# Optimization experiments

Hardware: AMD Instinct MI355X
Metric: run time of the kernel (lower is better)

Reference implementation:

```python
import jax, jax.numpy as jnp
import numpy as np

B, T, D = 8, 2048, 1024

def _xavier(key, shape):
    fan_in, fan_out = shape[1], shape[0]
    limit = float(np.sqrt(6.0 / (fan_in + fan_out)))
    return jax.random.uniform(key, shape, jnp.float32, -limit, limit)

def setup_inputs() -> dict:
    key = jax.random.key(0)
    ks = jax.random.split(key, 6)
    x = jax.random.normal(ks[0], (B, T, D), jnp.float32)
    return {
        "x": x,
        "h0": jnp.zeros((B, D), jnp.float32),
        "W_in": _xavier(ks[1], (D, D)),      # in_proj.weight [d_inner, dim]
        "W_alpha": _xavier(ks[2], (D, D)),
        "d_alpha": jnp.full((D,), 0.1, jnp.float32),
        "b_alpha": jnp.full((D,), 2.0, jnp.float32),
        "W_x": _xavier(ks[3], (D, D)),
        "b_v": jnp.zeros((D,), jnp.float32),
        "W_out": _xavier(ks[4], (D, D)),     # out_proj.weight [dim, d_inner]
    }

def _silu(u):
    return u * jax.nn.sigmoid(u)

def reference(x, h0, W_in, W_alpha, d_alpha, b_alpha, W_x, b_v, W_out):
    # in_proj + SiLU: [B,T,D]
    x_proj = _silu(jnp.einsum('btd,ed->bte', x, W_in))
    # to [T,B,D] for the scan
    x_rnn = jnp.transpose(x_proj, (1, 0, 2))
    # precompute per-step gate/value GEMM contributions (as in torch ref)
    alpha_x = jnp.einsum('tbd,ed->tbe', x_rnn, W_alpha)          # [T,B,D]
    v_all = jnp.tanh(jnp.einsum('tbd,ed->tbe', x_rnn, W_x) + b_v)  # [T,B,D]

    def step(h_prev, inputs):
        ax_t, v_t = inputs
        alpha = jax.nn.sigmoid(ax_t + d_alpha * h_prev + b_alpha)
        h_new = alpha * h_prev + (1.0 - alpha) * v_t
        out_t = h_new * _silu(h_new)
        return h_new, out_t

    h_final, cell_out = jax.lax.scan(step, h0, (alpha_x, v_all))  # cell_out: [T,B,D]
    cell_out = jnp.transpose(cell_out, (1, 0, 2))                 # [B,T,D]
    output = jnp.einsum('btd,ed->bte', cell_out, W_out)
    return output, h_final
```

## Files before the change

kernel.cpp:

```cpp
#include <hip/hip_runtime.h>
#include <hip/hip_bf16.h>

typedef __attribute__((ext_vector_type(8))) short short8;
typedef __attribute__((ext_vector_type(4))) short short4v;
typedef __attribute__((ext_vector_type(4))) float f32x4;

#define Dk 1024
#define TT 2048
#define BB 8
#define MROWS (BB * TT)
#define LOG2E 1.44269504088896f

#if defined(__has_builtin)
#if __has_builtin(__builtin_amdgcn_rcpf)
#define FAST_RCP(x) __builtin_amdgcn_rcpf(x)
#endif
#if __has_builtin(__builtin_amdgcn_exp2f)
#define FAST_EXP2(x) __builtin_amdgcn_exp2f(x)
#endif
#endif
#ifndef FAST_RCP
#define FAST_RCP(x) (1.f / (x))
#endif
#ifndef FAST_EXP2
#define FAST_EXP2(x) exp2f(x)
#endif

__device__ __forceinline__ void gload_lds16(const void* g, void* l) {
    __builtin_amdgcn_global_load_lds(
        (const __attribute__((address_space(1))) void*)g,
        (__attribute__((address_space(3))) void*)l, 16, 0, 0);
}

__device__ __forceinline__ float sigmoidf_fast(float x) {
    return FAST_RCP(1.f + FAST_EXP2(-x * LOG2E));
}

__device__ __forceinline__ unsigned short bf16_bits(float x) {
    union { __hip_bfloat16 h; unsigned short u; } c;
    c.h = __float2bfloat16(x);
    return c.u;
}

__global__ __launch_bounds__(256)
void cvt_all(const float* __restrict__ x,
             const float* __restrict__ w0, const float* __restrict__ w1,
             const float* __restrict__ w2, const float* __restrict__ w3,
             __hip_bfloat16* __restrict__ xo,
             __hip_bfloat16* __restrict__ o0, __hip_bfloat16* __restrict__ o1,
             __hip_bfloat16* __restrict__ o2, __hip_bfloat16* __restrict__ o3)
{
    const int bid = blockIdx.x;
    const float* in;
    __hip_bfloat16* out;
    int base;
    if (bid < 16384) {
        in = x; out = xo; base = bid * 1024;
    } else {
        const int wbid  = bid - 16384;
        const int which = wbid >> 10;
        in  = which == 0 ? w0 : which == 1 ? w1 : which == 2 ? w2 : w3;
        out = which == 0 ? o0 : which == 1 ? o1 : which == 2 ? o2 : o3;
        base = (wbid & 1023) * 1024;
    }
    const int i = base + threadIdx.x * 4;
    const float4 v = *(const float4*)(in + i);
    __hip_bfloat16 tmp[4];
    tmp[0] = __float2bfloat16(v.x);
    tmp[1] = __float2bfloat16(v.y);
    tmp[2] = __float2bfloat16(v.z);
    tmp[3] = __float2bfloat16(v.w);
    *(short4v*)(out + i) = *(const short4v*)tmp;
}

template<int EPI>
__global__ __launch_bounds__(512, 2)
void gemm256(const __hip_bfloat16* __restrict__ A,
             const __hip_bfloat16* __restrict__ Bw,
             const float* __restrict__ bias,
             void* __restrict__ CoutV)
{
    __shared__ __align__(16) char lds[3 * 32768];

    const int tid  = threadIdx.x;
    const int bid  = blockIdx.x;
    const int nbid = (bid & 7) * 32 + (bid >> 3);
    const int tn   = nbid & 3;
    const int tm   = nbid >> 2;
    const int lane = tid & 63;
    const int w    = tid >> 6;
    const int wm   = w >> 2;
    const int wn   = w & 3;
    const int l15  = lane & 15;
    const int lq   = lane >> 4;

    const size_t baseA = (size_t)(tm * 256) * Dk;
    const size_t baseB = (size_t)(tn * 256) * Dk;

    int offA[8], offB[4];
#pragma unroll
    for (int m = 0; m < 8; ++m) {
        const int row = wm * 128 + m * 16 + l15;
        offA[m] = (row * 4 + (lq ^ (row & 3))) * 16;
    }
#pragma unroll
    for (int n = 0; n < 4; ++n) {
        const int row = wn * 64 + n * 16 + l15;
        offB[n] = 16384 + (row * 4 + (lq ^ (row & 3))) * 16;
    }

    auto stagePh = [&](int kt, char* dst, int phase) {
#pragma unroll
        for (int j = 0; j < 2; ++j) {
            const int slot = (phase * 2 + j) * 512 + tid;
            const int s    = slot & 1023;
            const int row  = s >> 2;
            const int cb   = (s & 3) ^ (row & 3);
            const __hip_bfloat16* src =
                ((slot >> 10) ? Bw + baseB : A + baseA)
                + (size_t)row * Dk + kt * 32 + cb * 8;
            gload_lds16(src, dst + slot * 16);
        }
    };

    f32x4 acc[8][4];
#pragma unroll
    for (int m = 0; m < 8; ++m)
#pragma unroll
        for (int n = 0; n < 4; ++n)
            acc[m][n] = (f32x4){0.f, 0.f, 0.f, 0.f};

    char* b0 = lds;
    char* b1 = lds + 32768;
    char* b2 = lds + 65536;

    stagePh(0, b0, 0); stagePh(0, b0, 1);
    stagePh(1, b1, 0); stagePh(1, b1, 1);
    asm volatile("s_waitcnt vmcnt(4)" ::: "memory");
    __builtin_amdgcn_s_barrier();

    char* cbuf = b0;
    char* nbuf = b1;
    char* sbuf = b2;

    for (int t = 0; t < 32; ++t) {
        short8 af[4], af2[4], bfr[4];

#pragma unroll
        for (int n = 0; n < 4; ++n)
            bfr[n] = *(const short8*)(cbuf + offB[n]);
#pragma unroll
        for (int m = 0; m < 4; ++m)
            af[m] = *(const short8*)(cbuf + offA[m]);
        if (t < 30) stagePh(t + 2, sbuf, 0);
        __builtin_amdgcn_s_barrier();
        __builtin_amdgcn_s_setprio(1);
#pragma unroll
        for (int m = 0; m < 4; ++m)
#pragma unroll
            for (int n = 0; n < 4; ++n)
                acc[m][n] = __builtin_amdgcn_mfma_f32_16x16x32_bf16(
                    af[m], bfr[n], acc[m][n], 0, 0, 0);
        __builtin_amdgcn_s_setprio(0);
        __builtin_amdgcn_s_barrier();

#pragma unroll
        for (int m = 0; m < 4; ++m)
            af2[m] = *(const short8*)(cbuf + offA[4 + m]);
        if (t < 30) stagePh(t + 2, sbuf, 1);
        __builtin_amdgcn_s_barrier();
        __builtin_amdgcn_s_setprio(1);
#pragma unroll
        for (int m = 0; m < 4; ++m)
#pragma unroll
            for (int n = 0; n < 4; ++n)
                acc[4 + m][n] = __builtin_amdgcn_mfma_f32_16x16x32_bf16(
                    af2[m], bfr[n], acc[4 + m][n], 0, 0, 0);
        __builtin_amdgcn_s_setprio(0);

        if (t < 30) {
            asm volatile("s_waitcnt vmcnt(4)" ::: "memory");
        } else if (t == 30) {
            asm volatile("s_waitcnt vmcnt(0)" ::: "memory");
        }
        if (t < 31) __builtin_amdgcn_s_barrier();

        char* tmp = cbuf; cbuf = nbuf; nbuf = sbuf; sbuf = tmp;
    }

#pragma unroll
    for (int m = 0; m < 8; ++m) {
#pragma unroll
        for (int n = 0; n < 4; ++n) {
            const int col = tn * 256 + wn * 64 + n * 16 + l15;
            float bv_ = 0.f;
            if (EPI == 6 || EPI == 7) bv_ = bias[col];
#pragma unroll
            for (int j = 0; j < 4; ++j) {
                const int rowg = tm * 256 + wm * 128 + m * 16 + lq * 4 + j;
                const size_t idx = (size_t)rowg * Dk + col;
                const float xv = acc[m][n][j];
                if constexpr (EPI == 0) {
                    ((__hip_bfloat16*)CoutV)[idx] =
                        __float2bfloat16(xv * sigmoidf_fast(xv));
                } else if constexpr (EPI == 1) {
                    ((float*)CoutV)[idx] = xv;
                } else if constexpr (EPI == 6) {
                    const float e = FAST_EXP2(-(xv + bv_) * LOG2E);
                    ((unsigned short*)CoutV)[idx * 2] = bf16_bits(e);
                } else {
                    const float y = xv + bv_;
                    const float e = FAST_EXP2(fabsf(y) * (2.f * LOG2E));
                    float tv = 1.f - 2.f * FAST_RCP(e + 1.f);
                    tv = copysignf(tv, y);
                    ((unsigned short*)CoutV)[idx * 2 + 1] = bf16_bits(tv);
                }
            }
        }
    }
}

__global__ __launch_bounds__(128)
void scan_kernel(const unsigned int* __restrict__ EV,
                 const float* __restrict__ h0,
                 const float* __restrict__ dal,
                 __hip_bfloat16* __restrict__ cell, float* __restrict__ hfin)
{
    constexpr int CH  = 32;
    constexpr int NCH = TT / CH;
    __shared__ __align__(16) unsigned int lEV[2][CH * 64];
    __shared__ __align__(16) float        lH [2][CH * 64];

    const int tid  = threadIdx.x;
    const int wave = tid >> 6;
    const int lane = tid & 63;
    const int bx   = blockIdx.x;
    const int b    = bx >> 4;
    const int d0   = (bx & 15) * 64;
    const int d    = d0 + lane;
    const int g    = b * Dk + d;

    float nl2 = -dal[d] * LOG2E;
    if (fabsf(nl2) < 1e-18f) nl2 = -1e-18f;
    const float inv_nl2 = 1.f / nl2;

    const size_t sbase = (size_t)b * TT * Dk + d0;

    if (wave == 0) {
        float ht = h0[g] * nl2;

        const int sl = lane >> 4;
        const int co = (lane & 15) * 4;
        auto issue = [&](int ck, int buf) {
#pragma unroll
            for (int grp = 0; grp < 8; ++grp) {
                const size_t off = sbase + (size_t)(ck * CH + grp * 4 + sl) * Dk + co;
                gload_lds16(EV + off, (void*)&lEV[buf][grp * 256]);
            }
        };

        issue(0, 0);
        asm volatile("s_waitcnt vmcnt(0)" ::: "memory");
        __builtin_amdgcn_sched_barrier(0);

        for (int k = 0; k < NCH; ++k) {
            const int buf = k & 1;
            if (k + 1 < NCH) issue(k + 1, buf ^ 1);
            __builtin_amdgcn_sched_barrier(0);

#pragma unroll
            for (int s = 0; s < CH; ++s) {
                const unsigned int wv = lEV[buf][s * 64 + lane];
                const float E  = __uint_as_float(wv << 16);
                const float Vt = __uint_as_float(wv & 0xffff0000u) * nl2;
                const float u  = FAST_EXP2(ht);
                const float al = FAST_RCP(fmaf(E, u, 1.f));
                ht = fmaf(al, ht - Vt, Vt);
                lH[buf][s * 64 + lane] = ht;
            }
            __builtin_amdgcn_sched_barrier(0);
            asm volatile("s_waitcnt vmcnt(0) lgkmcnt(0)" ::: "memory");
            __builtin_amdgcn_sched_barrier(0);
            __builtin_amdgcn_s_barrier();
        }
        hfin[g] = ht * inv_nl2;
    } else {
        for (int k = 0; k < NCH; ++k) {
            __builtin_amdgcn_s_barrier();
            __builtin_amdgcn_sched_barrier(0);
            const int buf = k & 1;
            const size_t cbase = sbase + (size_t)(k * CH) * Dk + lane;
#pragma unroll
            for (int s = 0; s < CH; ++s) {
                const float ht = lH[buf][s * 64 + lane];
                const float h  = ht * inv_nl2;
                const float sg = FAST_RCP(1.f + FAST_EXP2(-h * LOG2E));
                cell[cbase + (size_t)s * Dk] = __float2bfloat16(h * h * sg);
            }
        }
    }
}

extern "C" void kernel_launch(void* const* d_in, const int* in_sizes, int n_in,
                              void* d_out, int out_size, void* d_ws, size_t ws_size,
                              hipStream_t stream)
{
    const float* x     = (const float*)d_in[0];
    const float* h0    = (const float*)d_in[1];
    const float* W_in  = (const float*)d_in[2];
    const float* W_al  = (const float*)d_in[3];
    const float* d_al  = (const float*)d_in[4];
    const float* b_al  = (const float*)d_in[5];
    const float* W_x   = (const float*)d_in[6];
    const float* b_v   = (const float*)d_in[7];
    const float* W_out = (const float*)d_in[8];

    float* out  = (float*)d_out;
    float* hfin = out + (size_t)MROWS * Dk;

    char* ws = (char*)d_ws;
    const size_t bfBuf = (size_t)MROWS * Dk * sizeof(__hip_bfloat16);
    const size_t wBuf  = (size_t)Dk * Dk * sizeof(__hip_bfloat16);

    __hip_bfloat16* xb    = (__hip_bfloat16*)(ws);
    __hip_bfloat16* Winb  = (__hip_bfloat16*)(ws + bfBuf);
    __hip_bfloat16* Walb  = (__hip_bfloat16*)(ws + bfBuf + wBuf);
    __hip_bfloat16* Wxb   = (__hip_bfloat16*)(ws + bfBuf + 2 * wBuf);
    __hip_bfloat16* Woutb = (__hip_bfloat16*)(ws + bfBuf + 3 * wBuf);
    char* rest = ws + bfBuf + 4 * wBuf;
    __hip_bfloat16* xproj = (__hip_bfloat16*)rest;
    unsigned int*   EVb   = (unsigned int*)(rest + bfBuf);

    __hip_bfloat16* cellb = xproj;

    dim3 blk(256);
    cvt_all<<<dim3(16384 + 4096), blk, 0, stream>>>(
        x, W_in, W_al, W_x, W_out, xb, Winb, Walb, Wxb, Woutb);

    dim3 ggrid(256), gblk(512);
    gemm256<0><<<ggrid, gblk, 0, stream>>>(xb,    Winb,  nullptr, xproj);
    gemm256<6><<<ggrid, gblk, 0, stream>>>(xproj, Walb,  b_al,    EVb);
    gemm256<7><<<ggrid, gblk, 0, stream>>>(xproj, Wxb,   b_v,     EVb);
    scan_kernel<<<dim3(128), dim3(128), 0, stream>>>(EVb, h0, d_al, cellb, hfin);
    gemm256<1><<<ggrid, gblk, 0, stream>>>(cellb, Woutb, nullptr, out);
}
```

Measured before the change: 276.7 us.

## Fuse alpha/value GEMMs, restructure GEMM main loop, widen scan chunks

The alpha and value projections now run as one GEMM over concatenated weights, with 512 blocks and an epilogue that writes both halves of the packed EV buffer. That epilogue also folds the -d_alpha*log2e scale into V, which removes a multiply from the serial scan step. The GEMM main loop stages each full tile at once and runs all 32 MFMAs between barriers, dropping the two-phase split and the min-blocks launch bound. The scan doubles its chunk to 64 steps and uses two consumer waves to split the output writes. This trades fewer launches and barriers for more register pressure and possibly lower occupancy in the GEMM.

```diff
diff --git a/kernel.cpp b/kernel.cpp
--- a/kernel.cpp
+++ b/kernel.cpp
@@ -73,20 +73,25 @@
     *(short4v*)(out + i) = *(const short4v*)tmp;
 }
 
-template<int EPI>
-__global__ __launch_bounds__(512, 2)
+template<int EPI, int TNW>
+__global__ __launch_bounds__(512)
 void gemm256(const __hip_bfloat16* __restrict__ A,
-             const __hip_bfloat16* __restrict__ Bw,
-             const float* __restrict__ bias,
+             const __hip_bfloat16* __restrict__ B1,
+             const __hip_bfloat16* __restrict__ B2,
+             const float* __restrict__ bias1,
+             const float* __restrict__ bias2,
+             const float* __restrict__ dal,
              void* __restrict__ CoutV)
 {
     __shared__ __align__(16) char lds[3 * 32768];
 
+    constexpr int SH = (TNW == 4) ? 2 : 3;
     const int tid  = threadIdx.x;
     const int bid  = blockIdx.x;
-    const int nbid = (bid & 7) * 32 + (bid >> 3);
-    const int tn   = nbid & 3;
-    const int tm   = nbid >> 2;
+    const int cpx  = (64 * TNW) >> 3;
+    const int nbid = (bid & 7) * cpx + (bid >> 3);
+    const int tn   = nbid & (TNW - 1);
+    const int tm   = nbid >> SH;
     const int lane = tid & 63;
     const int w    = tid >> 6;
     const int wm   = w >> 2;
@@ -95,7 +100,10 @@
     const int lq   = lane >> 4;
 
     const size_t baseA = (size_t)(tm * 256) * Dk;
-    const size_t baseB = (size_t)(tn * 256) * Dk;
+    const __hip_bfloat16* Bp;
+    if (TNW == 8) Bp = (tn < 4) ? B1 + (size_t)(tn * 256) * Dk
+                                : B2 + (size_t)((tn - 4) * 256) * Dk;
+    else          Bp = B1 + (size_t)(tn * 256) * Dk;
 
     int offA[8], offB[4];
 #pragma unroll
@@ -109,15 +117,15 @@
         offB[n] = 16384 + (row * 4 + (lq ^ (row & 3))) * 16;
     }
 
-    auto stagePh = [&](int kt, char* dst, int phase) {
-#pragma unroll
-        for (int j = 0; j < 2; ++j) {
-            const int slot = (phase * 2 + j) * 512 + tid;
+    auto stageTile = [&](int kt, char* dst) {
+#pragma unroll
+        for (int j = 0; j < 4; ++j) {
+            const int slot = j * 512 + tid;
             const int s    = slot & 1023;
             const int row  = s >> 2;
             const int cb   = (s & 3) ^ (row & 3);
             const __hip_bfloat16* src =
-                ((slot >> 10) ? Bw + baseB : A + baseA)
+                ((slot >> 10) ? Bp : A + baseA)
                 + (size_t)row * Dk + kt * 32 + cb * 8;
             gload_lds16(src, dst + slot * 16);
         }
@@ -130,53 +138,34 @@
         for (int n = 0; n < 4; ++n)
             acc[m][n] = (f32x4){0.f, 0.f, 0.f, 0.f};
 
-    char* b0 = lds;
-    char* b1 = lds + 32768;
-    char* b2 = lds + 65536;
-
-    stagePh(0, b0, 0); stagePh(0, b0, 1);
-    stagePh(1, b1, 0); stagePh(1, b1, 1);
+    char* cbuf = lds;
+    char* nbuf = lds + 32768;
+    char* sbuf = lds + 65536;
+
+    stageTile(0, cbuf);
+    stageTile(1, nbuf);
     asm volatile("s_waitcnt vmcnt(4)" ::: "memory");
     __builtin_amdgcn_s_barrier();
 
-    char* cbuf = b0;
-    char* nbuf = b1;
-    char* sbuf = b2;
-
     for (int t = 0; t < 32; ++t) {
-        short8 af[4], af2[4], bfr[4];
-
+        if (t < 30) stageTile(t + 2, sbuf);
+
+        short8 af[8], bfr[4];
 #pragma unroll
         for (int n = 0; n < 4; ++n)
             bfr[n] = *(const short8*)(cbuf + offB[n]);
 #pragma unroll
-        for (int m = 0; m < 4; ++m)
+        for (int m = 0; m < 8; ++m)
             af[m] = *(const short8*)(cbuf + offA[m]);
-        if (t < 30) stagePh(t + 2, sbuf, 0);
-        __builtin_amdgcn_s_barrier();
+
         __builtin_amdgcn_s_setprio(1);
 #pragma unroll
-        for (int m = 0; m < 4; ++m)
+        for (int m = 0; m < 8; ++m)
 #pragma unroll
             for (int n = 0; n < 4; ++n)
                 acc[m][n] = __builtin_amdgcn_mfma_f32_16x16x32_bf16(
                     af[m], bfr[n], acc[m][n], 0, 0, 0);
         __builtin_amdgcn_s_setprio(0);
-        __builtin_amdgcn_s_barrier();
-
-#pragma unroll
-        for (int m = 0; m < 4; ++m)
-            af2[m] = *(const short8*)(cbuf + offA[4 + m]);
-        if (t < 30) stagePh(t + 2, sbuf, 1);
-        __builtin_amdgcn_s_barrier();
-        __builtin_amdgcn_s_setprio(1);
-#pragma unroll
-        for (int m = 0; m < 4; ++m)
-#pragma unroll
-            for (int n = 0; n < 4; ++n)
-                acc[4 + m][n] = __builtin_amdgcn_mfma_f32_16x16x32_bf16(
-                    af2[m], bfr[n], acc[4 + m][n], 0, 0, 0);
-        __builtin_amdgcn_s_setprio(0);
 
         if (t < 30) {
             asm volatile("s_waitcnt vmcnt(4)" ::: "memory");
@@ -193,40 +182,45 @@
 #pragma unroll
         for (int n = 0; n < 4; ++n) {
             const int col = tn * 256 + wn * 64 + n * 16 + l15;
-            float bv_ = 0.f;
-            if (EPI == 6 || EPI == 7) bv_ = bias[col];
 #pragma unroll
             for (int j = 0; j < 4; ++j) {
                 const int rowg = tm * 256 + wm * 128 + m * 16 + lq * 4 + j;
-                const size_t idx = (size_t)rowg * Dk + col;
                 const float xv = acc[m][n][j];
                 if constexpr (EPI == 0) {
+                    const size_t idx = (size_t)rowg * Dk + col;
                     ((__hip_bfloat16*)CoutV)[idx] =
                         __float2bfloat16(xv * sigmoidf_fast(xv));
                 } else if constexpr (EPI == 1) {
+                    const size_t idx = (size_t)rowg * Dk + col;
                     ((float*)CoutV)[idx] = xv;
-                } else if constexpr (EPI == 6) {
-                    const float e = FAST_EXP2(-(xv + bv_) * LOG2E);
-                    ((unsigned short*)CoutV)[idx * 2] = bf16_bits(e);
                 } else {
-                    const float y = xv + bv_;
-                    const float e = FAST_EXP2(fabsf(y) * (2.f * LOG2E));
-                    float tv = 1.f - 2.f * FAST_RCP(e + 1.f);
-                    tv = copysignf(tv, y);
-                    ((unsigned short*)CoutV)[idx * 2 + 1] = bf16_bits(tv);
+                    const int dcol = col & 1023;
+                    const size_t idx = (size_t)rowg * Dk + dcol;
+                    if (col < 1024) {
+                        const float e = FAST_EXP2(-(xv + bias1[dcol]) * LOG2E);
+                        ((unsigned short*)CoutV)[idx * 2] = bf16_bits(e);
+                    } else {
+                        const float y = xv + bias2[dcol];
+                        const float e = FAST_EXP2(fabsf(y) * (2.f * LOG2E));
+                        float tv = 1.f - 2.f * FAST_RCP(e + 1.f);
+                        tv = copysignf(tv, y);
+                        float nl2 = -dal[dcol] * LOG2E;
+                        if (fabsf(nl2) < 1e-18f) nl2 = -1e-18f;
+                        ((unsigned short*)CoutV)[idx * 2 + 1] = bf16_bits(tv * nl2);
+                    }
                 }
             }
         }
     }
 }
 
-__global__ __launch_bounds__(128)
+__global__ __launch_bounds__(192)
 void scan_kernel(const unsigned int* __restrict__ EV,
                  const float* __restrict__ h0,
                  const float* __restrict__ dal,
                  __hip_bfloat16* __restrict__ cell, float* __restrict__ hfin)
 {
-    constexpr int CH  = 32;
+    constexpr int CH  = 64;
     constexpr int NCH = TT / CH;
     __shared__ __align__(16) unsigned int lEV[2][CH * 64];
     __shared__ __align__(16) float        lH [2][CH * 64];
@@ -253,18 +247,16 @@
         const int co = (lane & 15) * 4;
         auto issue = [&](int ck, int buf) {
 #pragma unroll
-            for (int grp = 0; grp < 8; ++grp) {
+            for (int grp = 0; grp < 16; ++grp) {
                 const size_t off = sbase + (size_t)(ck * CH + grp * 4 + sl) * Dk + co;
                 gload_lds16(EV + off, (void*)&lEV[buf][grp * 256]);
             }
         };
 
         issue(0, 0);
-        asm volatile("s_waitcnt vmcnt(0)" ::: "memory");
-        __builtin_amdgcn_sched_barrier(0);
-
         for (int k = 0; k < NCH; ++k) {
             const int buf = k & 1;
+            asm volatile("s_waitcnt vmcnt(0)" ::: "memory");
             if (k + 1 < NCH) issue(k + 1, buf ^ 1);
             __builtin_amdgcn_sched_barrier(0);
 
@@ -272,26 +264,25 @@
             for (int s = 0; s < CH; ++s) {
                 const unsigned int wv = lEV[buf][s * 64 + lane];
                 const float E  = __uint_as_float(wv << 16);
-                const float Vt = __uint_as_float(wv & 0xffff0000u) * nl2;
+                const float Vt = __uint_as_float(wv & 0xffff0000u);
                 const float u  = FAST_EXP2(ht);
                 const float al = FAST_RCP(fmaf(E, u, 1.f));
                 ht = fmaf(al, ht - Vt, Vt);
                 lH[buf][s * 64 + lane] = ht;
             }
-            __builtin_amdgcn_sched_barrier(0);
-            asm volatile("s_waitcnt vmcnt(0) lgkmcnt(0)" ::: "memory");
-            __builtin_amdgcn_sched_barrier(0);
+            asm volatile("s_waitcnt lgkmcnt(0)" ::: "memory");
             __builtin_amdgcn_s_barrier();
         }
         hfin[g] = ht * inv_nl2;
     } else {
+        const int s0 = (wave - 1) * 32;
         for (int k = 0; k < NCH; ++k) {
             __builtin_amdgcn_s_barrier();
-            __builtin_amdgcn_sched_barrier(0);
             const int buf = k & 1;
             const size_t cbase = sbase + (size_t)(k * CH) * Dk + lane;
 #pragma unroll
-            for (int s = 0; s < CH; ++s) {
+            for (int si = 0; si < 32; ++si) {
+                const int s = s0 + si;
                 const float ht = lH[buf][s * 64 + lane];
                 const float h  = ht * inv_nl2;
                 const float sg = FAST_RCP(1.f + FAST_EXP2(-h * LOG2E));
@@ -337,10 +328,12 @@
     cvt_all<<<dim3(16384 + 4096), blk, 0, stream>>>(
         x, W_in, W_al, W_x, W_out, xb, Winb, Walb, Wxb, Woutb);
 
-    dim3 ggrid(256), gblk(512);
-    gemm256<0><<<ggrid, gblk, 0, stream>>>(xb,    Winb,  nullptr, xproj);
-    gemm256<6><<<ggrid, gblk, 0, stream>>>(xproj, Walb,  b_al,    EVb);
-    gemm256<7><<<ggrid, gblk, 0, stream>>>(xproj, Wxb,   b_v,     EVb);
-    scan_kernel<<<dim3(128), dim3(128), 0, stream>>>(EVb, h0, d_al, cellb, hfin);
-    gemm256<1><<<ggrid, gblk, 0, stream>>>(cellb, Woutb, nullptr, out);
-}
+    dim3 gblk(512);
+    gemm256<0, 4><<<dim3(256), gblk, 0, stream>>>(
+        xb, Winb, nullptr, nullptr, nullptr, nullptr, xproj);
+    gemm256<8, 8><<<dim3(512), gblk, 0, stream>>>(
+        xproj, Walb, Wxb, b_al, b_v, d_al, EVb);
+    scan_kernel<<<dim3(128), dim3(192), 0, stream>>>(EVb, h0, d_al, cellb, hfin);
+    gemm256<1, 4><<<dim3(256), gblk, 0, stream>>>(
+        cellb, Woutb, nullptr, nullptr, nullptr, nullptr, out);
+}
```

After: 285.0 us. 3.0% more time.
